# Optimization experiments

Measured on AMD Instinct MI355X. Metric: run time of the kernel, lower is better.

## Reference

```python
import jax, jax.numpy as jnp
import numpy as np

B, T, DQ, DV, A, F, K = 64, 1024, 1024, 512, 512, 32, 31


def setup_inputs() -> dict:
    key = jax.random.key(0)
    ks = jax.random.split(key, 8)
    query = jax.random.normal(ks[0], (B, DQ), jnp.float32)
    values = jax.random.normal(ks[1], (B, T, DV), jnp.float32)
    # decoder-step states (as produced by init_states)
    attention_cum = jnp.zeros((B, T), jnp.float32)
    attention_old = jnp.zeros((B, T), jnp.float32)
    alpha = jnp.concatenate([jnp.ones((B, 1), jnp.float32),
                             jnp.zeros((B, T - 1), jnp.float32) + 1e-7], axis=1)
    # learned parameters (Glorot-ish scaling)
    W_query = jax.random.normal(ks[2], (DQ, A), jnp.float32) / np.sqrt(DQ)
    W_inputs = jax.random.normal(ks[3], (DV, A), jnp.float32) / np.sqrt(DV)
    v_w = jax.random.normal(ks[4], (A, 1), jnp.float32) / np.sqrt(A)
    v_b = jnp.zeros((1,), jnp.float32)
    loc_kernel = jax.random.normal(ks[5], (K, 2, F), jnp.float32) / np.sqrt(K * 2)  # WIO
    W_loc = jax.random.normal(ks[6], (F, A), jnp.float32) / np.sqrt(F)
    return {"query": query, "values": values, "attention_cum": attention_cum,
            "attention_old": attention_old, "alpha": alpha,
            "W_query": W_query, "W_inputs": W_inputs, "v_w": v_w, "v_b": v_b,
            "loc_kernel": loc_kernel, "W_loc": W_loc}


def reference(query, values, attention_cum, attention_old, alpha,
              W_query, W_inputs, v_w, v_b, loc_kernel, W_loc):
    # process_values: cached projection of encoder memory  [B,T,A]
    processed_values = jnp.einsum('btd,da->bta', values, W_inputs)
    # location features: conv over stacked (old, cum) attention  [B,T,2]->[B,T,F]
    attn_cat = jnp.stack([attention_old, attention_cum], axis=2)
    conv = jax.lax.conv_general_dilated(attn_cat, loc_kernel, window_strides=(1,),
                                        padding='SAME',
                                        dimension_numbers=('NWC', 'WIO', 'NWC'))
    processed_attn = jnp.einsum('btf,fa->bta', conv, W_loc)
    # query projection  [B,1,A]
    processed_query = (query @ W_query)[:, None, :]
    # additive score  [B,T]
    score = (jnp.tanh(processed_values + processed_query + processed_attn) @ v_w)[..., 0] + v_b
    scores_norm = jax.nn.softmax(score, axis=-1)
    # forward attention recursion
    fwd_shifted = jnp.pad(alpha[:, :-1], ((0, 0), (1, 0)))
    new_alpha = (0.5 * alpha + 0.5 * fwd_shifted + 1e-8) * scores_norm
    new_alpha = new_alpha / jnp.sum(new_alpha, axis=1, keepdims=True)
    attn_weights = new_alpha
    # updated states
    new_cum = attention_cum + scores_norm
    new_old = attn_weights
    # context vector  [B,DV]
    context = jnp.einsum('bt,btd->bd', attn_weights, values)
    return (context, attn_weights, new_cum, new_old, new_alpha)
```

## Files before the change

### kernel.cpp

```cpp
#include <hip/hip_runtime.h>
#include <hip/hip_bf16.h>
#include <cstdint>
#include <cstddef>

#define B 64
#define T 1024
#define DQ 1024
#define DV 512
#define A_DIM 512
#define F_DIM 32
#define KW 31
#define M_TOT (B*T)
#define KEXT2 576
#define NCH 9

typedef __attribute__((ext_vector_type(8))) short short8;
typedef __attribute__((ext_vector_type(4))) short short4v;
typedef __attribute__((ext_vector_type(4))) float f32x4;

static __device__ __forceinline__ unsigned short f2bf(float f) {
    unsigned int u = __builtin_bit_cast(unsigned int, f);
    u += 0x7fffu + ((u >> 16) & 1u);
    return (unsigned short)(u >> 16);
}
static __device__ __forceinline__ float bf2f(unsigned short h) {
    return __builtin_bit_cast(float, (unsigned int)h << 16);
}
static __device__ __forceinline__ short8 pack8(float4 x0, float4 x1) {
    short8 pk;
    pk[0] = (short)f2bf(x0.x); pk[1] = (short)f2bf(x0.y);
    pk[2] = (short)f2bf(x0.z); pk[3] = (short)f2bf(x0.w);
    pk[4] = (short)f2bf(x1.x); pk[5] = (short)f2bf(x1.y);
    pk[6] = (short)f2bf(x1.z); pk[7] = (short)f2bf(x1.w);
    return pk;
}
static __device__ __forceinline__ float tanh_fast(float x) {
    float e = __expf(2.0f * x);
    return 1.0f - 2.0f * __builtin_amdgcn_rcpf(e + 1.0f);
}

#define LDSDMA16(gptr, lptr)                                                        \
    __builtin_amdgcn_global_load_lds(                                               \
        (const __attribute__((address_space(1))) void*)(const void*)(gptr),         \
        (__attribute__((address_space(3))) void*)(void*)(lptr), 16, 0, 0)

__global__ void prep_kernel(const float* __restrict__ values,
                            const float* __restrict__ query, const float* __restrict__ Wq,
                            const float* __restrict__ Wi, const float* __restrict__ Wl,
                            const float* __restrict__ old_, const float* __restrict__ cum_,
                            const float* __restrict__ lk,
                            unsigned short* __restrict__ vbf, float* __restrict__ pq,
                            float* __restrict__ score, unsigned short* __restrict__ Bt,
                            unsigned short* __restrict__ convb) {
    __shared__ __align__(16) char smem[16640];
    int bid = blockIdx.x, tid = threadIdx.x;
    if (bid < 4096) {
        size_t base = (size_t)bid * 8192 + (size_t)tid * 8;
        #pragma unroll
        for (int j = 0; j < 4; ++j) {
            size_t idx = base + (size_t)j * 2048;
            float4 x0 = *(const float4*)(values + idx);
            float4 x1 = *(const float4*)(values + idx + 4);
            *(short8*)(vbf + idx) = pack8(x0, x1);
        }
    } else if (bid < 4608) {
        float (*red)[64] = (float(*)[64])smem;
        int pid = bid - 4096;
        int gid = pid * 256 + tid;
        if (gid < M_TOT) score[gid] = 0.f;
        int b = pid >> 3, a0 = (pid & 7) * 64;
        int al = tid & 63, ks = tid >> 6;
        const float* qr = query + (size_t)b * DQ + ks * 256;
        const float* wc = Wq + (size_t)(ks * 256) * A_DIM + a0 + al;
        float acc = 0.f;
        #pragma unroll 8
        for (int k = 0; k < 256; ++k) acc += qr[k] * wc[(size_t)k * A_DIM];
        red[ks][al] = acc;
        __syncthreads();
        if (ks == 0)
            pq[b * A_DIM + a0 + al] = red[0][al] + red[1][al] + red[2][al] + red[3][al];
    } else if (bid < 4680) {
        float (*tile)[65] = (float(*)[65])smem;
        int tb = bid - 4608;
        if (tb < 64) {
            int k0 = (tb >> 3) * 64, a0 = (tb & 7) * 64;
            int al = tid & 63, ko = tid >> 6;
            #pragma unroll
            for (int j = 0; j < 16; ++j) {
                int kl = j * 4 + ko;
                tile[kl][al] = Wi[(size_t)(k0 + kl) * A_DIM + a0 + al];
            }
            __syncthreads();
            int kl2 = tid & 63, ao = tid >> 6;
            #pragma unroll
            for (int j = 0; j < 16; ++j) {
                int al2 = j * 4 + ao;
                Bt[(size_t)(a0 + al2) * KEXT2 + k0 + kl2] = f2bf(tile[kl2][al2]);
            }
        } else {
            int a0 = (tb - 64) * 64;
            int al = tid & 63, ko = tid >> 6;
            #pragma unroll
            for (int j = 0; j < 8; ++j) {
                int kl = j * 4 + ko;
                tile[kl][al] = Wl[(size_t)kl * A_DIM + a0 + al];
            }
            __syncthreads();
            int kl2 = tid & 31, ao = tid >> 5;
            #pragma unroll
            for (int j = 0; j < 8; ++j) {
                int al2 = j * 8 + ao;
                Bt[(size_t)(a0 + al2) * KEXT2 + DV + kl2] = f2bf(tile[kl2][al2]);
            }
            #pragma unroll
            for (int j = 0; j < 8; ++j) {
                int idx = j * 256 + tid;
                int a_l = idx >> 5, kp = idx & 31;
                Bt[(size_t)(a0 + a_l) * KEXT2 + 544 + kp] = 0;
            }
        }
    } else {
        float* sOld = (float*)smem;
        float* sCum = sOld + 94;
        float* sLK  = sCum + 94;
        int cid = bid - 4680;
        int b = cid >> 4, t0 = (cid & 15) * 64;
        int tl = tid & 63, fg = tid >> 6;
        for (int j = tid; j < 94; j += 256) {
            int tt = t0 - 15 + j;
            bool ok = (tt >= 0 && tt < T);
            sOld[j] = ok ? old_[b * T + tt] : 0.f;
            sCum[j] = ok ? cum_[b * T + tt] : 0.f;
        }
        for (int j = tid; j < KW * 2 * F_DIM; j += 256) sLK[j] = lk[j];
        __syncthreads();
        float acc[8];
        #pragma unroll
        for (int f = 0; f < 8; ++f) acc[f] = 0.f;
        for (int k = 0; k < KW; ++k) {
            float o = sOld[tl + k], c = sCum[tl + k];
            const float* lo = &sLK[(k * 2 + 0) * F_DIM + fg * 8];
            const float* lc = &sLK[(k * 2 + 1) * F_DIM + fg * 8];
            #pragma unroll
            for (int f = 0; f < 8; ++f) acc[f] += o * lo[f] + c * lc[f];
        }
        short8 pk;
        #pragma unroll
        for (int f = 0; f < 8; ++f) pk[f] = (short)f2bf(acc[f]);
        unsigned short* dst = convb + (size_t)(b * T + t0 + tl) * 64 + fg * 8;
        *(short8*)dst = pk;
        *(short8*)(dst + 32) = (short8)0;
    }
}

template<bool VBF>
__launch_bounds__(256, 3)
__global__ void gemm_score(const float* __restrict__ values,
                           const unsigned short* __restrict__ vbf,
                           const unsigned short* __restrict__ Bt,
                           const unsigned short* __restrict__ convb,
                           const float* __restrict__ pq,
                           const float* __restrict__ vw,
                           float* __restrict__ score) {
    __shared__ __align__(16) short sA[128 * 64];
    __shared__ __align__(16) short sB[128 * 64];
    __shared__ float sPQ[128];
    __shared__ float sVW[128];
    int tid = threadIdx.x;
    int x = blockIdx.x & 7, l = blockIdx.x >> 3;
    int mt = x * 64 + (l >> 2), nq = l & 3;
    int m0 = mt * 128, n0 = nq * 128;
    int b = m0 >> 10;
    if (tid < 128) { sPQ[tid] = pq[b * A_DIM + n0 + tid]; sVW[tid] = vw[n0 + tid]; }
    int w = tid >> 6, lane = tid & 63, q = lane >> 4, l15 = lane & 15;
    int wm = w & 1, wn = w >> 1;
    f32x4 acc[4][4];
    #pragma unroll
    for (int mi = 0; mi < 4; ++mi)
        #pragma unroll
        for (int ni = 0; ni < 4; ++ni) acc[mi][ni] = (f32x4)0.f;

    for (int c = 0; c < NCH; ++c) {
        __syncthreads();
        #pragma unroll
        for (int j = 0; j < 4; ++j) {
            int slot = j * 256 + tid;
            int row = slot >> 3, seg = ((slot & 7) - row) & 7;
            const unsigned short* gB = Bt + (size_t)(n0 + row) * KEXT2 + c * 64 + seg * 8;
            LDSDMA16(gB, &sB[(j * 256 + w * 64) * 8]);
        }
        if (VBF) {
            #pragma unroll
            for (int j = 0; j < 4; ++j) {
                int slot = j * 256 + tid;
                int row = slot >> 3, seg = ((slot & 7) - row) & 7;
                const unsigned short* gA = (c < 8)
                    ? vbf + (size_t)(m0 + row) * DV + c * 64 + seg * 8
                    : convb + (size_t)(m0 + row) * 64 + seg * 8;
                LDSDMA16(gA, &sA[(j * 256 + w * 64) * 8]);
            }
        } else {
            #pragma unroll
            for (int jj = 0; jj < 4; ++jj) {
                int slot = tid * 4 + jj;
                int row = slot >> 3, sl = slot & 7, seg = (sl - row) & 7;
                short8 pk;
                if (c < 8) {
                    const float* s0 = values + (size_t)(m0 + row) * DV + c * 64 + seg * 8;
                    pk = pack8(*(const float4*)s0, *(const float4*)(s0 + 4));
                } else {
                    pk = *(const short8*)(convb + (size_t)(m0 + row) * 64 + seg * 8);
                }
                *(short8*)&sA[slot * 8] = pk;
            }
        }
        __syncthreads();
        #pragma unroll
        for (int h = 0; h < 2; ++h) {
            short8 af[4], bfr[4];
            int sgl = h * 4 + q;
            #pragma unroll
            for (int mi = 0; mi < 4; ++mi) {
                int r = wm * 64 + mi * 16 + l15;
                af[mi] = *(const short8*)&sA[r * 64 + (((sgl + r) & 7) << 3)];
            }
            #pragma unroll
            for (int ni = 0; ni < 4; ++ni) {
                int r = wn * 64 + ni * 16 + l15;
                bfr[ni] = *(const short8*)&sB[r * 64 + (((sgl + r) & 7) << 3)];
            }
            #pragma unroll
            for (int mi = 0; mi < 4; ++mi)
                #pragma unroll
                for (int ni = 0; ni < 4; ++ni)
                    acc[mi][ni] = __builtin_amdgcn_mfma_f32_16x16x32_bf16(af[mi], bfr[ni], acc[mi][ni], 0, 0, 0);
        }
    }
    #pragma unroll
    for (int mi = 0; mi < 4; ++mi) {
        #pragma unroll
        for (int r = 0; r < 4; ++r) {
            float s = 0.f;
            #pragma unroll
            for (int ni = 0; ni < 4; ++ni) {
                int col = wn * 64 + ni * 16 + l15;
                float xv = acc[mi][ni][r] + sPQ[col];
                s += tanh_fast(xv) * sVW[col];
            }
            #pragma unroll
            for (int off = 1; off < 16; off <<= 1) s += __shfl_xor(s, off, 64);
            if (l15 == 0)
                atomicAdd(&score[m0 + wm * 64 + mi * 16 + q * 4 + r], s);
        }
    }
}

__global__ void softmax_fwd(const float* __restrict__ score,
                            const float* __restrict__ alpha,
                            const float* __restrict__ cum,
                            float* __restrict__ out) {
    int b = blockIdx.x, t = threadIdx.x;
    __shared__ float sred[16];
    __shared__ float sbc;
    float sc = score[b * T + t];
    int wid = t >> 6, lane = t & 63;
    float m = sc;
    #pragma unroll
    for (int off = 32; off; off >>= 1) m = fmaxf(m, __shfl_xor(m, off, 64));
    if (lane == 0) sred[wid] = m;
    __syncthreads();
    if (t == 0) { float mm = sred[0]; for (int i = 1; i < 16; ++i) mm = fmaxf(mm, sred[i]); sbc = mm; }
    __syncthreads();
    float M = sbc;
    float e = __expf(sc - M);
    float s = e;
    #pragma unroll
    for (int off = 32; off; off >>= 1) s += __shfl_xor(s, off, 64);
    __syncthreads();
    if (lane == 0) sred[wid] = s;
    __syncthreads();
    if (t == 0) { float ss = 0.f; for (int i = 0; i < 16; ++i) ss += sred[i]; sbc = ss; }
    __syncthreads();
    float sn = e / sbc;
    float a_t = alpha[b * T + t];
    float a_p = (t > 0) ? alpha[b * T + t - 1] : 0.f;
    float ua = (0.5f * (a_t + a_p) + 1e-8f) * sn;
    float u = ua;
    #pragma unroll
    for (int off = 32; off; off >>= 1) u += __shfl_xor(u, off, 64);
    __syncthreads();
    if (lane == 0) sred[wid] = u;
    __syncthreads();
    if (t == 0) { float ss = 0.f; for (int i = 0; i < 16; ++i) ss += sred[i]; sbc = ss; }
    __syncthreads();
    float wgt = ua / sbc;
    float* attnw  = out + B * DV;
    float* ncum   = attnw + B * T;
    float* nold   = ncum + B * T;
    float* nalpha = nold + B * T;
    attnw[b * T + t]  = wgt;
    ncum[b * T + t]   = cum[b * T + t] + sn;
    nold[b * T + t]   = wgt;
    nalpha[b * T + t] = wgt;
    if (t < DV) out[b * DV + t] = 0.f;
}

__global__ void context_kernel(const float* __restrict__ values,
                               const unsigned short* __restrict__ vbf,
                               int use_bf, float* __restrict__ out) {
    __shared__ float red[4][256];
    const float* attnw = out + B * DV;
    int b = blockIdx.x >> 3, tq = (blockIdx.x >> 1) & 3, dh = blockIdx.x & 1;
    int sub = threadIdx.x >> 6, dg = threadIdx.x & 63;
    int t0 = tq * 256 + sub * 64;
    int d0 = dh * 256 + dg * 4;
    float acc[4];
    #pragma unroll
    for (int f = 0; f < 4; ++f) acc[f] = 0.f;
    if (use_bf) {
        for (int tt = 0; tt < 64; ++tt) {
            int t = t0 + tt;
            float wgt = attnw[b * T + t];
            short4v v = *(const short4v*)(vbf + (size_t)(b * T + t) * DV + d0);
            #pragma unroll
            for (int f = 0; f < 4; ++f) acc[f] += wgt * bf2f((unsigned short)v[f]);
        }
    } else {
        for (int tt = 0; tt < 64; ++tt) {
            int t = t0 + tt;
            float wgt = attnw[b * T + t];
            float4 xv = *(const float4*)(values + (size_t)(b * T + t) * DV + d0);
            acc[0] += wgt * xv.x; acc[1] += wgt * xv.y;
            acc[2] += wgt * xv.z; acc[3] += wgt * xv.w;
        }
    }
    #pragma unroll
    for (int f = 0; f < 4; ++f) red[sub][dg * 4 + f] = acc[f];
    __syncthreads();
    if (sub == 0) {
        #pragma unroll
        for (int f = 0; f < 4; ++f) {
            int di = dg * 4 + f;
            float s = red[0][di] + red[1][di] + red[2][di] + red[3][di];
            atomicAdd(&out[b * DV + dh * 256 + di], s);
        }
    }
}

extern "C" void kernel_launch(void* const* d_in, const int* in_sizes, int n_in,
                              void* d_out, int out_size, void* d_ws, size_t ws_size,
                              hipStream_t stream) {
    const float* query  = (const float*)d_in[0];
    const float* values = (const float*)d_in[1];
    const float* cum    = (const float*)d_in[2];
    const float* old_   = (const float*)d_in[3];
    const float* alpha  = (const float*)d_in[4];
    const float* Wq     = (const float*)d_in[5];
    const float* Wi     = (const float*)d_in[6];
    const float* vw     = (const float*)d_in[7];
    const float* lk     = (const float*)d_in[9];
    const float* Wl     = (const float*)d_in[10];
    float* out = (float*)d_out;
    char* ws = (char*)d_ws;
    float* ws_pq            = (float*)(ws);
    float* ws_score         = (float*)(ws + 131072);
    unsigned short* ws_Bt   = (unsigned short*)(ws + 393216);
    unsigned short* ws_conv = (unsigned short*)(ws + 1048576);
    unsigned short* ws_vbf  = (unsigned short*)(ws + 16777216);
    const bool big = ws_size >= (size_t)88080384;

    if (big) {
        prep_kernel<<<5704, 256, 0, stream>>>(values, query, Wq, Wi, Wl, old_, cum, lk,
                                              ws_vbf, ws_pq, ws_score, ws_Bt, ws_conv);
        gemm_score<true><<<2048, 256, 0, stream>>>(values, ws_vbf, ws_Bt, ws_conv, ws_pq, vw, ws_score);
    } else {
        prep_kernel<<<1608, 256, 0, stream>>>(values, query, Wq, Wi, Wl, old_, cum, lk,
                                              ws_vbf, ws_pq, ws_score, ws_Bt, ws_conv);
        gemm_score<false><<<2048, 256, 0, stream>>>(values, ws_vbf, ws_Bt, ws_conv, ws_pq, vw, ws_score);
    }
    softmax_fwd<<<64, 1024, 0, stream>>>(ws_score, alpha, cum, out);
    context_kernel<<<512, 256, 0, stream>>>(values, ws_vbf, big ? 1 : 0, out);
}
```

Measured before the change: 303.6 us.

## Drop bf16 values staging; convert fp32 values inline in GEMM and split prep kernel

Removes the pre-pass that converted the whole values tensor to bf16 in workspace and the LDS-DMA path that read it. The GEMM now always loads fp32 values and packs them to bf16 in registers before writing LDS, and context reads fp32 values directly. The fused prep kernel is split into separate pq, Bt-transpose and conv kernels. This saves a full write and re-read of a 64 MB bf16 copy. In exchange the GEMM reads twice the bytes per tile through registers instead of async DMA, and context reads fp32 instead of bf16.

Result: slower. 335.5 us (+10.5%).

```diff
diff --git a/kernel.cpp b/kernel.cpp
--- a/kernel.cpp
+++ b/kernel.cpp
@@ -15,16 +15,12 @@
 #define NCH 9
 
 typedef __attribute__((ext_vector_type(8))) short short8;
-typedef __attribute__((ext_vector_type(4))) short short4v;
 typedef __attribute__((ext_vector_type(4))) float f32x4;
 
 static __device__ __forceinline__ unsigned short f2bf(float f) {
     unsigned int u = __builtin_bit_cast(unsigned int, f);
     u += 0x7fffu + ((u >> 16) & 1u);
     return (unsigned short)(u >> 16);
-}
-static __device__ __forceinline__ float bf2f(unsigned short h) {
-    return __builtin_bit_cast(float, (unsigned int)h << 16);
 }
 static __device__ __forceinline__ short8 pack8(float4 x0, float4 x1) {
     short8 pk;
@@ -44,119 +40,106 @@
         (const __attribute__((address_space(1))) void*)(const void*)(gptr),         \
         (__attribute__((address_space(3))) void*)(void*)(lptr), 16, 0, 0)
 
-__global__ void prep_kernel(const float* __restrict__ values,
-                            const float* __restrict__ query, const float* __restrict__ Wq,
-                            const float* __restrict__ Wi, const float* __restrict__ Wl,
-                            const float* __restrict__ old_, const float* __restrict__ cum_,
-                            const float* __restrict__ lk,
-                            unsigned short* __restrict__ vbf, float* __restrict__ pq,
-                            float* __restrict__ score, unsigned short* __restrict__ Bt,
-                            unsigned short* __restrict__ convb) {
-    __shared__ __align__(16) char smem[16640];
-    int bid = blockIdx.x, tid = threadIdx.x;
-    if (bid < 4096) {
-        size_t base = (size_t)bid * 8192 + (size_t)tid * 8;
-        #pragma unroll
-        for (int j = 0; j < 4; ++j) {
-            size_t idx = base + (size_t)j * 2048;
-            float4 x0 = *(const float4*)(values + idx);
-            float4 x1 = *(const float4*)(values + idx + 4);
-            *(short8*)(vbf + idx) = pack8(x0, x1);
-        }
-    } else if (bid < 4608) {
-        float (*red)[64] = (float(*)[64])smem;
-        int pid = bid - 4096;
-        int gid = pid * 256 + tid;
-        if (gid < M_TOT) score[gid] = 0.f;
-        int b = pid >> 3, a0 = (pid & 7) * 64;
-        int al = tid & 63, ks = tid >> 6;
-        const float* qr = query + (size_t)b * DQ + ks * 256;
-        const float* wc = Wq + (size_t)(ks * 256) * A_DIM + a0 + al;
-        float acc = 0.f;
-        #pragma unroll 8
-        for (int k = 0; k < 256; ++k) acc += qr[k] * wc[(size_t)k * A_DIM];
-        red[ks][al] = acc;
+__global__ void pq_kernel(const float* __restrict__ query, const float* __restrict__ Wq,
+                          float* __restrict__ pq, float* __restrict__ score) {
+    __shared__ float red[8][32];
+    int gid = blockIdx.x * 256 + threadIdx.x;
+    if (gid < M_TOT) score[gid] = 0.f;
+    int b = blockIdx.x >> 4, a0 = (blockIdx.x & 15) * 32;
+    int al = threadIdx.x & 31, ks = threadIdx.x >> 5;
+    const float* qr = query + (size_t)b * DQ + ks * 128;
+    const float* wc = Wq + (size_t)(ks * 128) * A_DIM + a0 + al;
+    float acc = 0.f;
+    #pragma unroll 8
+    for (int k = 0; k < 128; ++k) acc += qr[k] * wc[(size_t)k * A_DIM];
+    red[ks][al] = acc;
+    __syncthreads();
+    if (ks == 0) {
+        float s = 0.f;
+        #pragma unroll
+        for (int j = 0; j < 8; ++j) s += red[j][al];
+        pq[b * A_DIM + a0 + al] = s;
+    }
+}
+
+__global__ void bt_kernel(const float* __restrict__ Wi, const float* __restrict__ Wl,
+                          unsigned short* __restrict__ Bt) {
+    __shared__ float tile[64][65];
+    int tid = threadIdx.x;
+    if (blockIdx.x < 64) {
+        int k0 = (blockIdx.x >> 3) * 64, a0 = (blockIdx.x & 7) * 64;
+        int al = tid & 63, ko = tid >> 6;
+        #pragma unroll
+        for (int j = 0; j < 16; ++j) {
+            int kl = j * 4 + ko;
+            tile[kl][al] = Wi[(size_t)(k0 + kl) * A_DIM + a0 + al];
+        }
         __syncthreads();
-        if (ks == 0)
-            pq[b * A_DIM + a0 + al] = red[0][al] + red[1][al] + red[2][al] + red[3][al];
-    } else if (bid < 4680) {
-        float (*tile)[65] = (float(*)[65])smem;
-        int tb = bid - 4608;
-        if (tb < 64) {
-            int k0 = (tb >> 3) * 64, a0 = (tb & 7) * 64;
-            int al = tid & 63, ko = tid >> 6;
-            #pragma unroll
-            for (int j = 0; j < 16; ++j) {
-                int kl = j * 4 + ko;
-                tile[kl][al] = Wi[(size_t)(k0 + kl) * A_DIM + a0 + al];
-            }
-            __syncthreads();
-            int kl2 = tid & 63, ao = tid >> 6;
-            #pragma unroll
-            for (int j = 0; j < 16; ++j) {
-                int al2 = j * 4 + ao;
-                Bt[(size_t)(a0 + al2) * KEXT2 + k0 + kl2] = f2bf(tile[kl2][al2]);
-            }
-        } else {
-            int a0 = (tb - 64) * 64;
-            int al = tid & 63, ko = tid >> 6;
-            #pragma unroll
-            for (int j = 0; j < 8; ++j) {
-                int kl = j * 4 + ko;
-                tile[kl][al] = Wl[(size_t)kl * A_DIM + a0 + al];
-            }
-            __syncthreads();
-            int kl2 = tid & 31, ao = tid >> 5;
-            #pragma unroll
-            for (int j = 0; j < 8; ++j) {
-                int al2 = j * 8 + ao;
-                Bt[(size_t)(a0 + al2) * KEXT2 + DV + kl2] = f2bf(tile[kl2][al2]);
-            }
-            #pragma unroll
-            for (int j = 0; j < 8; ++j) {
-                int idx = j * 256 + tid;
-                int a_l = idx >> 5, kp = idx & 31;
-                Bt[(size_t)(a0 + a_l) * KEXT2 + 544 + kp] = 0;
-            }
+        int kl2 = tid & 63, ao = tid >> 6;
+        #pragma unroll
+        for (int j = 0; j < 16; ++j) {
+            int al2 = j * 4 + ao;
+            Bt[(size_t)(a0 + al2) * KEXT2 + k0 + kl2] = f2bf(tile[kl2][al2]);
         }
     } else {
-        float* sOld = (float*)smem;
-        float* sCum = sOld + 94;
-        float* sLK  = sCum + 94;
-        int cid = bid - 4680;
-        int b = cid >> 4, t0 = (cid & 15) * 64;
-        int tl = tid & 63, fg = tid >> 6;
-        for (int j = tid; j < 94; j += 256) {
-            int tt = t0 - 15 + j;
-            bool ok = (tt >= 0 && tt < T);
-            sOld[j] = ok ? old_[b * T + tt] : 0.f;
-            sCum[j] = ok ? cum_[b * T + tt] : 0.f;
-        }
-        for (int j = tid; j < KW * 2 * F_DIM; j += 256) sLK[j] = lk[j];
+        int a0 = (blockIdx.x - 64) * 64;
+        int al = tid & 63, ko = tid >> 6;
+        #pragma unroll
+        for (int j = 0; j < 8; ++j) {
+            int kl = j * 4 + ko;
+            tile[kl][al] = Wl[(size_t)kl * A_DIM + a0 + al];
+        }
         __syncthreads();
-        float acc[8];
-        #pragma unroll
-        for (int f = 0; f < 8; ++f) acc[f] = 0.f;
-        for (int k = 0; k < KW; ++k) {
-            float o = sOld[tl + k], c = sCum[tl + k];
-            const float* lo = &sLK[(k * 2 + 0) * F_DIM + fg * 8];
-            const float* lc = &sLK[(k * 2 + 1) * F_DIM + fg * 8];
-            #pragma unroll
-            for (int f = 0; f < 8; ++f) acc[f] += o * lo[f] + c * lc[f];
-        }
-        short8 pk;
-        #pragma unroll
-        for (int f = 0; f < 8; ++f) pk[f] = (short)f2bf(acc[f]);
-        unsigned short* dst = convb + (size_t)(b * T + t0 + tl) * 64 + fg * 8;
-        *(short8*)dst = pk;
-        *(short8*)(dst + 32) = (short8)0;
-    }
-}
-
-template<bool VBF>
+        int kl2 = tid & 31, ao = tid >> 5;
+        #pragma unroll
+        for (int j = 0; j < 8; ++j) {
+            int al2 = j * 8 + ao;
+            Bt[(size_t)(a0 + al2) * KEXT2 + DV + kl2] = f2bf(tile[kl2][al2]);
+        }
+        #pragma unroll
+        for (int j = 0; j < 8; ++j) {
+            int idx = j * 256 + tid;
+            int a_l = idx >> 5, kp = idx & 31;
+            Bt[(size_t)(a0 + a_l) * KEXT2 + 544 + kp] = 0;
+        }
+    }
+}
+
+__global__ void conv_kernel(const float* __restrict__ old_, const float* __restrict__ cum_,
+                            const float* __restrict__ lk, unsigned short* __restrict__ convb) {
+    __shared__ float sOld[94], sCum[94];
+    __shared__ float sLK[KW * 2 * F_DIM];
+    int b = blockIdx.x >> 4, t0 = (blockIdx.x & 15) * 64;
+    int tid = threadIdx.x;
+    int tl = tid & 63, fg = tid >> 6;
+    for (int j = tid; j < 94; j += 256) {
+        int tt = t0 - 15 + j;
+        bool ok = (tt >= 0 && tt < T);
+        sOld[j] = ok ? old_[b * T + tt] : 0.f;
+        sCum[j] = ok ? cum_[b * T + tt] : 0.f;
+    }
+    for (int j = tid; j < KW * 2 * F_DIM; j += 256) sLK[j] = lk[j];
+    __syncthreads();
+    float acc[8];
+    #pragma unroll
+    for (int f = 0; f < 8; ++f) acc[f] = 0.f;
+    for (int k = 0; k < KW; ++k) {
+        float o = sOld[tl + k], c = sCum[tl + k];
+        const float* lo = &sLK[(k * 2 + 0) * F_DIM + fg * 8];
+        const float* lc = &sLK[(k * 2 + 1) * F_DIM + fg * 8];
+        #pragma unroll
+        for (int f = 0; f < 8; ++f) acc[f] += o * lo[f] + c * lc[f];
+    }
+    short8 pk;
+    #pragma unroll
+    for (int f = 0; f < 8; ++f) pk[f] = (short)f2bf(acc[f]);
+    unsigned short* dst = convb + (size_t)(b * T + t0 + tl) * 64 + fg * 8;
+    *(short8*)dst = pk;
+    *(short8*)(dst + 32) = (short8)0;
+}
+
 __launch_bounds__(256, 3)
 __global__ void gemm_score(const float* __restrict__ values,
-                           const unsigned short* __restrict__ vbf,
                            const unsigned short* __restrict__ Bt,
                            const unsigned short* __restrict__ convb,
                            const float* __restrict__ pq,
@@ -189,30 +172,18 @@
             const unsigned short* gB = Bt + (size_t)(n0 + row) * KEXT2 + c * 64 + seg * 8;
             LDSDMA16(gB, &sB[(j * 256 + w * 64) * 8]);
         }
-        if (VBF) {
-            #pragma unroll
-            for (int j = 0; j < 4; ++j) {
-                int slot = j * 256 + tid;
-                int row = slot >> 3, seg = ((slot & 7) - row) & 7;
-                const unsigned short* gA = (c < 8)
-                    ? vbf + (size_t)(m0 + row) * DV + c * 64 + seg * 8
-                    : convb + (size_t)(m0 + row) * 64 + seg * 8;
-                LDSDMA16(gA, &sA[(j * 256 + w * 64) * 8]);
+        #pragma unroll
+        for (int jj = 0; jj < 4; ++jj) {
+            int slot = tid * 4 + jj;
+            int row = slot >> 3, seg = ((slot & 7) - row) & 7;
+            short8 pk;
+            if (c < 8) {
+                const float* s0 = values + (size_t)(m0 + row) * DV + c * 64 + seg * 8;
+                pk = pack8(*(const float4*)s0, *(const float4*)(s0 + 4));
+            } else {
+                pk = *(const short8*)(convb + (size_t)(m0 + row) * 64 + seg * 8);
             }
-        } else {
-            #pragma unroll
-            for (int jj = 0; jj < 4; ++jj) {
-                int slot = tid * 4 + jj;
-                int row = slot >> 3, sl = slot & 7, seg = (sl - row) & 7;
-                short8 pk;
-                if (c < 8) {
-                    const float* s0 = values + (size_t)(m0 + row) * DV + c * 64 + seg * 8;
-                    pk = pack8(*(const float4*)s0, *(const float4*)(s0 + 4));
-                } else {
-                    pk = *(const short8*)(convb + (size_t)(m0 + row) * 64 + seg * 8);
-                }
-                *(short8*)&sA[slot * 8] = pk;
-            }
+            *(short8*)&sA[slot * 8] = pk;
         }
         __syncthreads();
         #pragma unroll
@@ -305,9 +276,7 @@
     if (t < DV) out[b * DV + t] = 0.f;
 }
 
-__global__ void context_kernel(const float* __restrict__ values,
-                               const unsigned short* __restrict__ vbf,
-                               int use_bf, float* __restrict__ out) {
+__global__ void context_kernel(const float* __restrict__ values, float* __restrict__ out) {
     __shared__ float red[4][256];
     const float* attnw = out + B * DV;
     int b = blockIdx.x >> 3, tq = (blockIdx.x >> 1) & 3, dh = blockIdx.x & 1;
@@ -317,22 +286,12 @@
     float acc[4];
     #pragma unroll
     for (int f = 0; f < 4; ++f) acc[f] = 0.f;
-    if (use_bf) {
-        for (int tt = 0; tt < 64; ++tt) {
-            int t = t0 + tt;
-            float wgt = attnw[b * T + t];
-            short4v v = *(const short4v*)(vbf + (size_t)(b * T + t) * DV + d0);
-            #pragma unroll
-            for (int f = 0; f < 4; ++f) acc[f] += wgt * bf2f((unsigned short)v[f]);
-        }
-    } else {
-        for (int tt = 0; tt < 64; ++tt) {
-            int t = t0 + tt;
-            float wgt = attnw[b * T + t];
-            float4 xv = *(const float4*)(values + (size_t)(b * T + t) * DV + d0);
-            acc[0] += wgt * xv.x; acc[1] += wgt * xv.y;
-            acc[2] += wgt * xv.z; acc[3] += wgt * xv.w;
-        }
+    for (int tt = 0; tt < 64; ++tt) {
+        int t = t0 + tt;
+        float wgt = attnw[b * T + t];
+        float4 xv = *(const float4*)(values + (size_t)(b * T + t) * DV + d0);
+        acc[0] += wgt * xv.x; acc[1] += wgt * xv.y;
+        acc[2] += wgt * xv.z; acc[3] += wgt * xv.w;
     }
     #pragma unroll
     for (int f = 0; f < 4; ++f) red[sub][dg * 4 + f] = acc[f];
@@ -366,18 +325,11 @@
     float* ws_score         = (float*)(ws + 131072);
     unsigned short* ws_Bt   = (unsigned short*)(ws + 393216);
     unsigned short* ws_conv = (unsigned short*)(ws + 1048576);
-    unsigned short* ws_vbf  = (unsigned short*)(ws + 16777216);
-    const bool big = ws_size >= (size_t)88080384;
-
-    if (big) {
-        prep_kernel<<<5704, 256, 0, stream>>>(values, query, Wq, Wi, Wl, old_, cum, lk,
-                                              ws_vbf, ws_pq, ws_score, ws_Bt, ws_conv);
-        gemm_score<true><<<2048, 256, 0, stream>>>(values, ws_vbf, ws_Bt, ws_conv, ws_pq, vw, ws_score);
-    } else {
-        prep_kernel<<<1608, 256, 0, stream>>>(values, query, Wq, Wi, Wl, old_, cum, lk,
-                                              ws_vbf, ws_pq, ws_score, ws_Bt, ws_conv);
-        gemm_score<false><<<2048, 256, 0, stream>>>(values, ws_vbf, ws_Bt, ws_conv, ws_pq, vw, ws_score);
-    }
+
+    pq_kernel<<<1024, 256, 0, stream>>>(query, Wq, ws_pq, ws_score);
+    bt_kernel<<<72, 256, 0, stream>>>(Wi, Wl, ws_Bt);
+    conv_kernel<<<1024, 256, 0, stream>>>(old_, cum, lk, ws_conv);
+    gemm_score<<<2048, 256, 0, stream>>>(values, ws_Bt, ws_conv, ws_pq, vw, ws_score);
     softmax_fwd<<<64, 1024, 0, stream>>>(ws_score, alpha, cum, out);
-    context_kernel<<<512, 256, 0, stream>>>(values, ws_vbf, big ? 1 : 0, out);
-}
+    context_kernel<<<512, 256, 0, stream>>>(values, out);
+}
```
